# Optimization experiments

Hardware: AMD Instinct MI355X
Metric: run time of the kernel (lower is better)

## Reference

```python
import jax, jax.numpy as jnp
import numpy as np

B, S, NU, ML, H, V = 32, 256, 4, 9, 768, 30522


def setup_inputs() -> dict:
    key = jax.random.key(0)
    ks = jax.random.split(key, 13)
    s = 1.0 / np.sqrt(H)
    return {
        "x": jax.random.randint(ks[0], (B, S), 0, V),
        "decoder_input": jax.random.normal(ks[1], (B, NU, H), jnp.float32) * 0.02,
        "encoder_output": jax.random.normal(ks[2], (B, S, H), jnp.float32) * 0.02,
        "hidden": jax.random.normal(ks[3], (1, B, H), jnp.float32) * 0.02,
        "max_len": ML,
        "teacher": jax.random.randint(ks[4], (B, NU, ML), 0, V),
        "embed_w": jax.random.normal(ks[5], (V, H), jnp.float32) * 0.02,
        "gru_w_ih": jax.random.uniform(ks[6], (3 * H, H), jnp.float32, -s, s),
        "gru_w_hh": jax.random.uniform(ks[7], (3 * H, H), jnp.float32, -s, s),
        "gru_b_ih": jax.random.uniform(ks[8], (3 * H,), jnp.float32, -s, s),
        "gru_b_hh": jax.random.uniform(ks[9], (3 * H,), jnp.float32, -s, s),
        "w_gen_w": jax.random.uniform(ks[10], (1, 3 * H), jnp.float32, -s, s),
        "w_gen_b": jax.random.uniform(ks[11], (1,), jnp.float32, -s, s),
    }


def reference(x, decoder_input, encoder_output, hidden, max_len, teacher,
              embed_w, gru_w_ih, gru_w_hh, gru_b_ih, gru_b_hh, w_gen_w, w_gen_b):
    pad_mask = (x == 0)                       # [B, S]
    b, nu, h_dim = decoder_input.shape
    h0 = hidden[0]                            # [B, H]

    # Teacher-forced input sequence for every (update, step): [NU*ML, B, H]
    tf = embed_w[teacher[:, :, :max_len - 1]]           # [B, NU, ML-1, H]
    tf = jnp.moveaxis(tf, 0, 2)                          # [NU, ML-1, B, H]
    first = jnp.swapaxes(decoder_input, 0, 1)[:, None]   # [NU, 1, B, H]
    ws = jnp.concatenate([first, tf], axis=1).reshape(nu * max_len, b, h_dim)

    def gru_cell(w, h):
        gi = w @ gru_w_ih.T + gru_b_ih        # [B, 3H]
        gh = h @ gru_w_hh.T + gru_b_hh
        i_r, i_z, i_n = jnp.split(gi, 3, axis=-1)
        h_r, h_z, h_n = jnp.split(gh, 3, axis=-1)
        r = jax.nn.sigmoid(i_r + h_r)
        z = jax.nn.sigmoid(i_z + h_z)
        n = jnp.tanh(i_n + r * h_n)
        return (1.0 - z) * n + z * h

    batch_idx = jnp.arange(b)[:, None]

    def step(h, w):
        h = gru_cell(w, h)                                    # [B, H]
        attn_e = jnp.einsum('bsh,bh->bs', encoder_output, h)  # [B, S]
        attn_e = jnp.where(pad_mask, -1e9, attn_e)
        attn_history = jax.nn.softmax(attn_e, axis=-1)        # [B, S]
        attn_vocab = jax.nn.softmax(h @ embed_w.T, axis=-1)   # [B, V]
        context = jnp.einsum('bs,bsh->bh', attn_history, encoder_output)
        gate_in = jnp.concatenate([w, h, context], axis=-1)   # [B, 3H]
        p_gen = jax.nn.sigmoid(gate_in @ w_gen_w.T + w_gen_b) # [B, 1]
        p_ctx = jnp.zeros_like(attn_vocab).at[batch_idx, x].add(attn_history)
        p_final = p_gen * attn_vocab + (1.0 - p_gen) * p_ctx  # [B, V]
        return h, p_final

    _, outs = jax.lax.scan(step, h0, ws)          # [NU*ML, B, V]
    outs = outs.reshape(nu, max_len, b, -1)       # [NU, ML, B, V]
    return jnp.transpose(outs, (2, 0, 1, 3))      # [B, NU, ML, V]
```

## Files before the change

kernel.cpp:

```cpp
#include <hip/hip_runtime.h>
#include <math.h>

#define BB_ 32
#define SS_ 256
#define HH_ 768
#define VV_ 30522
#define TT_ 36
#define MM_ 1152
#define NBLK_GRU 48

typedef __bf16 bf16x8 __attribute__((ext_vector_type(8)));
typedef __bf16 bf16x4 __attribute__((ext_vector_type(4)));
typedef float f32x4 __attribute__((ext_vector_type(4)));

__device__ __forceinline__ float sigmoidf_(float x) { return 1.f / (1.f + expf(-x)); }

__device__ __forceinline__ void async_load16(const void* g, void* l) {
  __builtin_amdgcn_global_load_lds(
      (const __attribute__((address_space(1))) void*)g,
      (__attribute__((address_space(3))) void*)l, 16, 0, 0);
}

__global__ __launch_bounds__(256) void cvt_bf16(const float* __restrict__ s,
                                                __bf16* __restrict__ d, int n4) {
  int i = blockIdx.x * 256 + threadIdx.x;
  if (i < n4) {
    float4 v = reinterpret_cast<const float4*>(s)[i];
    bf16x4 o;
    o[0] = (__bf16)v.x; o[1] = (__bf16)v.y; o[2] = (__bf16)v.z; o[3] = (__bf16)v.w;
    reinterpret_cast<bf16x4*>(d)[i] = o;
  }
}

__global__ __launch_bounds__(256) void build_ws(const float* __restrict__ dec,
                                                const int* __restrict__ teacher,
                                                const float* __restrict__ embed,
                                                __bf16* __restrict__ wsbf) {
  int idx = blockIdx.x * 256 + threadIdx.x;
  if (idx >= MM_ * HH_) return;
  int m = idx / HH_, k = idx - m * HH_;
  int tau = m >> 5, b = m & 31;
  int u = tau / 9, tt = tau - u * 9;
  float v;
  if (tt == 0) v = dec[((size_t)b * 4 + u) * HH_ + k];
  else v = embed[(size_t)teacher[(b * 4 + u) * 9 + tt - 1] * HH_ + k];
  wsbf[idx] = (__bf16)v;
}

__global__ __launch_bounds__(256) void enc_gate(const float* __restrict__ enc,
                                                const float* __restrict__ wgen,
                                                float* __restrict__ encg) {
  int row = blockIdx.x * 4 + (threadIdx.x >> 6);
  int lane = threadIdx.x & 63;
  const float* er = enc + (size_t)row * HH_;
  float ssum = 0.f;
#pragma unroll
  for (int i = 0; i < 12; ++i) ssum += er[i * 64 + lane] * wgen[1536 + i * 64 + lane];
  for (int off = 32; off; off >>= 1) ssum += __shfl_down(ssum, off);
  if (lane == 0) encg[row] = ssum;
}

template <int MODE>
__global__ __launch_bounds__(256) void gemm_bt2(const __bf16* __restrict__ A,
                                                const __bf16* __restrict__ Bm,
                                                float* __restrict__ C,
                                                float* __restrict__ rowsum,
                                                int Nreal, int ldC) {
  __shared__ __bf16 As[128 * 32];
  __shared__ __bf16 Bs[128 * 32];
  const int tid = threadIdx.x;
  const int lane = tid & 63, wave = tid >> 6;
  const int wm = wave >> 1, wn = wave & 1;
  const int q = lane >> 4, ln = lane & 15;
  const int m0 = blockIdx.y * 128, n0 = blockIdx.x * 128;
  const int srow = (wave << 5) + (lane >> 2);
  const int kc = lane & 3;
  const size_t aoff = (size_t)(m0 + srow) * HH_ + kc * 8;
  const size_t aoff2 = aoff + 16 * HH_;
  int br1 = n0 + srow;      if (br1 >= Nreal) br1 = Nreal - 1;
  int br2 = n0 + srow + 16; if (br2 >= Nreal) br2 = Nreal - 1;
  __bf16* lA1 = &As[srow * 32 + kc * 8];
  __bf16* lA2 = &As[(srow + 16) * 32 + kc * 8];
  __bf16* lB1 = &Bs[srow * 32 + kc * 8];
  __bf16* lB2 = &Bs[(srow + 16) * 32 + kc * 8];
  f32x4 acc[4][4] = {};
  for (int kb = 0; kb < 24; ++kb) {
    const int k0 = kb << 5;
    async_load16(A + aoff + k0, lA1);
    async_load16(A + aoff2 + k0, lA2);
    async_load16(Bm + (size_t)br1 * HH_ + kc * 8 + k0, lB1);
    async_load16(Bm + (size_t)br2 * HH_ + kc * 8 + k0, lB2);
    __syncthreads();
    bf16x8 af[4], bfr[4];
#pragma unroll
    for (int mi = 0; mi < 4; ++mi)
      af[mi] = *reinterpret_cast<const bf16x8*>(&As[(wm * 64 + mi * 16 + ln) * 32 + q * 8]);
#pragma unroll
    for (int ni = 0; ni < 4; ++ni)
      bfr[ni] = *reinterpret_cast<const bf16x8*>(&Bs[(wn * 64 + ni * 16 + ln) * 32 + q * 8]);
#pragma unroll
    for (int mi = 0; mi < 4; ++mi)
#pragma unroll
      for (int ni = 0; ni < 4; ++ni)
        acc[mi][ni] = __builtin_amdgcn_mfma_f32_16x16x32_bf16(af[mi], bfr[ni], acc[mi][ni], 0, 0, 0);
    __syncthreads();
  }
#pragma unroll
  for (int mi = 0; mi < 4; ++mi)
#pragma unroll
    for (int r2 = 0; r2 < 4; ++r2) {
      const int m = m0 + wm * 64 + mi * 16 + q * 4 + r2;
      if (MODE == 0) {
#pragma unroll
        for (int ni = 0; ni < 4; ++ni) {
          int n = n0 + wn * 64 + ni * 16 + ln;
          if (n < Nreal) C[(size_t)m * ldC + n] = acc[mi][ni][r2];
        }
      } else {
        float part = 0.f;
#pragma unroll
        for (int ni = 0; ni < 4; ++ni) {
          int n = n0 + wn * 64 + ni * 16 + ln;
          float e = expf(fminf(acc[mi][ni][r2], 60.f));
          if (n < Nreal) { C[(size_t)m * ldC + n] = e; part += e; }
        }
#pragma unroll
        for (int o = 1; o < 16; o <<= 1) part += __shfl_xor(part, o);
        if (ln == 0) atomicAdd(rowsum + m, part);
      }
    }
}

__global__ __launch_bounds__(128) void gru_scan(const __bf16* __restrict__ hid_bf,
                                                const float* __restrict__ H0,
                                                const __bf16* __restrict__ Whh,
                                                const float* __restrict__ GI,
                                                const float* __restrict__ bih,
                                                const float* __restrict__ bhh,
                                                __bf16* __restrict__ Ah,
                                                unsigned* __restrict__ flags) {
  __shared__ __bf16 WhhS[48 * HH_];
  const int tid = threadIdx.x, lane = tid & 63;
  const int mi = tid >> 6;
  const int q = lane >> 4, ln = lane & 15;
  const int jH = blockIdx.x * 16 + ln;
  for (int i = tid; i < 48 * 96; i += 128) {
    int row = i / 96, cs = i - row * 96;
    int g = row >> 4, jl = row & 15;
    bf16x8 v = *reinterpret_cast<const bf16x8*>(
        &Whh[((size_t)(g * 768 + blockIdx.x * 16 + jl)) * HH_ + cs * 8]);
    *reinterpret_cast<bf16x8*>(&WhhS[row * HH_ + ((cs ^ (row & 7)) * 8)]) = v;
  }
  const float bir = bih[jH], biz = bih[jH + 768], bin_ = bih[jH + 1536];
  const float bhr = bhh[jH], bhz = bhh[jH + 768], bhn = bhh[jH + 1536];
  float hc[4];
#pragma unroll
  for (int r2 = 0; r2 < 4; ++r2)
    hc[r2] = H0[(size_t)(mi * 16 + q * 4 + r2) * HH_ + jH];
  const __bf16* w0 = &WhhS[(0 + ln) * HH_];
  const __bf16* w1 = &WhhS[(16 + ln) * HH_];
  const __bf16* w2 = &WhhS[(32 + ln) * HH_];
  const int swz = (ln & 7) * 8;
  __syncthreads();
  for (int tau = 0; tau < TT_; ++tau) {
    const __bf16* arow = tau ? (Ah + ((size_t)(mi * 16 + ln) * TT_ + (tau - 1)) * HH_)
                             : (hid_bf + (size_t)(mi * 16 + ln) * HH_);
    const float* GIt = GI + (size_t)tau * BB_ * 2304;
    float gir[4], giz[4], gin[4];
#pragma unroll
    for (int r2 = 0; r2 < 4; ++r2) {
      const float* gi = GIt + (size_t)(mi * 16 + q * 4 + r2) * 2304;
      gir[r2] = gi[jH]; giz[r2] = gi[jH + 768]; gin[r2] = gi[jH + 1536];
    }
    f32x4 a0 = {}, a1 = {}, a2 = {};
#pragma unroll 4
    for (int kb = 0; kb < 24; ++kb) {
      int k0 = kb * 32 + q * 8;
      int kl = (k0 ^ swz);
      bf16x8 a = *reinterpret_cast<const bf16x8*>(arow + k0);
      bf16x8 b0 = *reinterpret_cast<const bf16x8*>(w0 + kl);
      bf16x8 b1 = *reinterpret_cast<const bf16x8*>(w1 + kl);
      bf16x8 b2 = *reinterpret_cast<const bf16x8*>(w2 + kl);
      a0 = __builtin_amdgcn_mfma_f32_16x16x32_bf16(a, b0, a0, 0, 0, 0);
      a1 = __builtin_amdgcn_mfma_f32_16x16x32_bf16(a, b1, a1, 0, 0, 0);
      a2 = __builtin_amdgcn_mfma_f32_16x16x32_bf16(a, b2, a2, 0, 0, 0);
    }
#pragma unroll
    for (int r2 = 0; r2 < 4; ++r2) {
      int b = mi * 16 + q * 4 + r2;
      float r = sigmoidf_(gir[r2] + bir + a0[r2] + bhr);
      float z = sigmoidf_(giz[r2] + biz + a1[r2] + bhz);
      float n = tanhf(gin[r2] + bin_ + r * (a2[r2] + bhn));
      float h = (1.f - z) * n + z * hc[r2];
      hc[r2] = h;
      Ah[((size_t)b * TT_ + tau) * HH_ + jH] = (__bf16)h;
    }
    if (tau < TT_ - 1) {
      __syncthreads();
      if (tid == 0)
        __hip_atomic_store(&flags[(size_t)blockIdx.x * 16], (unsigned)(tau + 1),
                           __ATOMIC_RELEASE, __HIP_MEMORY_SCOPE_AGENT);
      const unsigned tgt = (unsigned)(tau + 1);
      int ok = 0, spin = 0;
      while (!ok) {
        unsigned v = (lane < NBLK_GRU)
            ? __hip_atomic_load(&flags[(size_t)lane * 16], __ATOMIC_ACQUIRE,
                                __HIP_MEMORY_SCOPE_AGENT)
            : tgt;
        ok = __all((int)(v >= tgt));
        if (!ok) {
          __builtin_amdgcn_s_sleep(1);
          if (++spin > (1 << 20)) break;
        }
      }
    }
  }
}

__global__ __launch_bounds__(256) void attn_gemm(const __bf16* __restrict__ Ah,
                                                 const __bf16* __restrict__ encb,
                                                 float* __restrict__ E) {
  int b = blockIdx.x >> 2, stile = blockIdx.x & 3;
  int wave = threadIdx.x >> 6, lane = threadIdx.x & 63;
  int q = lane >> 4, ln = lane & 15;
  int s = stile * 64 + wave * 16 + ln;
  const __bf16* brow = encb + ((size_t)b * SS_ + s) * HH_;
  const __bf16* arow[3];
#pragma unroll
  for (int mt = 0; mt < 3; ++mt) {
    int tau = mt * 16 + ln; if (tau > 35) tau = 35;
    arow[mt] = Ah + ((size_t)b * TT_ + tau) * HH_;
  }
  f32x4 acc[3] = {};
#pragma unroll 4
  for (int kb = 0; kb < 24; ++kb) {
    int k0 = kb * 32 + q * 8;
    bf16x8 bb = *reinterpret_cast<const bf16x8*>(brow + k0);
#pragma unroll
    for (int mt = 0; mt < 3; ++mt) {
      bf16x8 aa = *reinterpret_cast<const bf16x8*>(arow[mt] + k0);
      acc[mt] = __builtin_amdgcn_mfma_f32_16x16x32_bf16(aa, bb, acc[mt], 0, 0, 0);
    }
  }
#pragma unroll
  for (int mt = 0; mt < 3; ++mt)
#pragma unroll
    for (int r2 = 0; r2 < 4; ++r2) {
      int tau = mt * 16 + q * 4 + r2;
      if (tau < 36) E[((size_t)b * TT_ + tau) * SS_ + s] = acc[mt][r2];
    }
}

__global__ __launch_bounds__(256) void softmax_pg(const float* __restrict__ E,
                                                  const int* __restrict__ x,
                                                  const float* __restrict__ encg,
                                                  const __bf16* __restrict__ wsbf,
                                                  const __bf16* __restrict__ Ah,
                                                  const float* __restrict__ wgen,
                                                  const float* __restrict__ wgenb,
                                                  float* __restrict__ attn,
                                                  float* __restrict__ pg) {
  int m = blockIdx.x;
  int b = m / TT_, tau = m - b * TT_;
  int m_in = tau * 32 + b;
  int t = threadIdx.x;
  __shared__ float red[256];
  __shared__ float r1[256], r2[256], r3[256];
  float e = E[(size_t)m * SS_ + t];
  if (x[b * SS_ + t] == 0) e = -1000000000.0f;
  red[t] = e; __syncthreads();
  for (int off = 128; off; off >>= 1) {
    if (t < off) red[t] = fmaxf(red[t], red[t + off]);
    __syncthreads();
  }
  float mx = red[0];
  float p = expf(e - mx);
  float dsum = 0.f;
#pragma unroll
  for (int i = 0; i < 3; ++i) {
    int k = t + i * 256;
    dsum += (float)wsbf[(size_t)m_in * HH_ + k] * wgen[k];
    dsum += (float)Ah[(size_t)m * HH_ + k] * wgen[768 + k];
  }
  float pe = p * encg[b * SS_ + t];
  r1[t] = p; r2[t] = pe; r3[t] = dsum; __syncthreads();
  for (int off = 128; off; off >>= 1) {
    if (t < off) { r1[t] += r1[t + off]; r2[t] += r2[t + off]; r3[t] += r3[t + off]; }
    __syncthreads();
  }
  float Z = r1[0];
  attn[(size_t)m * SS_ + t] = p / Z;
  if (t == 0) pg[m] = sigmoidf_(r3[0] + r2[0] / Z + wgenb[0]);
}

__global__ __launch_bounds__(256) void finalize(float* __restrict__ C,
                                                const float* __restrict__ rowsum,
                                                const float* __restrict__ pg) {
  int m = blockIdx.y;
  float scale = pg[m] / rowsum[m];
  int base_i = blockIdx.x * 2048;
  size_t rowb = (size_t)m * VV_;
#pragma unroll
  for (int j = 0; j < 8; ++j) {
    int i = base_i + j * 256 + threadIdx.x;
    if (i < VV_) C[rowb + i] *= scale;
  }
}

__global__ __launch_bounds__(256) void scatter_ctx(float* __restrict__ C,
                                                   const float* __restrict__ attn,
                                                   const float* __restrict__ pg,
                                                   const int* __restrict__ x) {
  int m = blockIdx.x, s = threadIdx.x;
  int b = m / TT_;
  float v = (1.f - pg[m]) * attn[(size_t)m * SS_ + s];
  int col = x[b * SS_ + s];
  atomicAdd(C + (size_t)m * VV_ + col, v);
}

extern "C" void kernel_launch(void* const* d_in, const int* in_sizes, int n_in,
                              void* d_out, int out_size, void* d_ws, size_t ws_size,
                              hipStream_t stream) {
  const int*   x       = (const int*)d_in[0];
  const float* dec     = (const float*)d_in[1];
  const float* enc     = (const float*)d_in[2];
  const float* hidden  = (const float*)d_in[3];
  const int*   teacher = (const int*)d_in[5];
  const float* embed   = (const float*)d_in[6];
  const float* wih     = (const float*)d_in[7];
  const float* whh     = (const float*)d_in[8];
  const float* bih     = (const float*)d_in[9];
  const float* bhh     = (const float*)d_in[10];
  const float* wgen    = (const float*)d_in[11];
  const float* wgenb   = (const float*)d_in[12];
  float* out = (float*)d_out;

  char* w = (char*)d_ws;
  __bf16* embed_bf = (__bf16*)w;  w += (size_t)VV_ * HH_ * 2;
  __bf16* enc_bf   = (__bf16*)w;  w += (size_t)BB_ * SS_ * HH_ * 2;
  __bf16* wih_bf   = (__bf16*)w;  w += (size_t)2304 * HH_ * 2;
  __bf16* whh_bf   = (__bf16*)w;  w += (size_t)2304 * HH_ * 2;
  __bf16* ws_bf    = (__bf16*)w;  w += (size_t)MM_ * HH_ * 2;
  __bf16* hid_bf   = (__bf16*)w;  w += (size_t)BB_ * HH_ * 2;
  __bf16* A_h      = (__bf16*)w;  w += (size_t)MM_ * HH_ * 2;
  float*  GI       = (float*)w;   w += (size_t)MM_ * 2304 * 4;
  float*  E        = (float*)w;   w += (size_t)MM_ * SS_ * 4;
  float*  attn     = (float*)w;   w += (size_t)MM_ * SS_ * 4;
  float*  encg     = (float*)w;   w += (size_t)BB_ * SS_ * 4;
  float*  pg       = (float*)w;   w += 8192;
  char*   ctl      = w;           w += 8192;
  float*    rowsum = (float*)ctl;
  unsigned* flags  = (unsigned*)(ctl + 4864);

  hipMemsetAsync(ctl, 0, 8192, stream);

  cvt_bf16<<<(VV_ * HH_ / 4 + 255) / 256, 256, 0, stream>>>(embed, embed_bf, VV_ * HH_ / 4);
  cvt_bf16<<<(BB_ * SS_ * HH_ / 4 + 255) / 256, 256, 0, stream>>>(enc, enc_bf, BB_ * SS_ * HH_ / 4);
  cvt_bf16<<<(2304 * HH_ / 4 + 255) / 256, 256, 0, stream>>>(wih, wih_bf, 2304 * HH_ / 4);
  cvt_bf16<<<(2304 * HH_ / 4 + 255) / 256, 256, 0, stream>>>(whh, whh_bf, 2304 * HH_ / 4);
  cvt_bf16<<<(BB_ * HH_ / 4 + 255) / 256, 256, 0, stream>>>(hidden, hid_bf, BB_ * HH_ / 4);

  build_ws<<<(MM_ * HH_ + 255) / 256, 256, 0, stream>>>(dec, teacher, embed, ws_bf);

  gemm_bt2<0><<<dim3(2304 / 128, MM_ / 128), 256, 0, stream>>>(ws_bf, wih_bf, GI, nullptr, 2304, 2304);

  enc_gate<<<BB_ * SS_ / 4, 256, 0, stream>>>(enc, wgen, encg);

  gru_scan<<<NBLK_GRU, 128, 0, stream>>>(hid_bf, hidden, whh_bf, GI, bih, bhh, A_h, flags);

  attn_gemm<<<BB_ * 4, 256, 0, stream>>>(A_h, enc_bf, E);
  softmax_pg<<<MM_, 256, 0, stream>>>(E, x, encg, ws_bf, A_h, wgen, wgenb, attn, pg);

  gemm_bt2<1><<<dim3((VV_ + 127) / 128, MM_ / 128), 256, 0, stream>>>(A_h, embed_bf, out, rowsum, VV_, VV_);

  finalize<<<dim3((VV_ + 2047) / 2048, MM_), 256, 0, stream>>>(out, rowsum, pg);
  scatter_ctx<<<MM_, 256, 0, stream>>>(out, attn, pg, x);
}
```

Measured before the change: 786.2 us.

## Cut GRU scan step latency with compact exchange buffer and prefetch

The recurrent GRU scan now exchanges the hidden state between blocks through a small double-buffered Hx array, written as packed 32-bit atomic stores, instead of reading back from the strided Ah output. The next step's input-gate values are prefetched before the inter-block spin-wait, the whole A row is loaded into registers before the MFMA loop, and the flag store and load become relaxed with a single acquire fence after the wait. The aim is to shorten the serial per-step critical path of the 36-step scan. Dropping release semantics on the flag store without an explicit release fence could let the Hx stores become visible after the flag, and the larger register footprint adds register pressure.

```diff
diff --git a/kernel.cpp b/kernel.cpp
--- a/kernel.cpp
+++ b/kernel.cpp
@@ -131,14 +131,15 @@
     }
 }
 
-__global__ __launch_bounds__(128) void gru_scan(const __bf16* __restrict__ hid_bf,
-                                                const float* __restrict__ H0,
-                                                const __bf16* __restrict__ Whh,
-                                                const float* __restrict__ GI,
-                                                const float* __restrict__ bih,
-                                                const float* __restrict__ bhh,
-                                                __bf16* __restrict__ Ah,
-                                                unsigned* __restrict__ flags) {
+__global__ __launch_bounds__(128, 1) void gru_scan(const __bf16* __restrict__ hid_bf,
+                                                   const float* __restrict__ H0,
+                                                   const __bf16* __restrict__ Whh,
+                                                   const float* __restrict__ GI,
+                                                   const float* __restrict__ bih,
+                                                   const float* __restrict__ bhh,
+                                                   __bf16* __restrict__ Ah,
+                                                   __bf16* __restrict__ Hx,
+                                                   unsigned* __restrict__ flags) {
   __shared__ __bf16 WhhS[48 * HH_];
   const int tid = threadIdx.x, lane = tid & 63;
   const int mi = tid >> 6;
@@ -161,30 +162,32 @@
   const __bf16* w1 = &WhhS[(16 + ln) * HH_];
   const __bf16* w2 = &WhhS[(32 + ln) * HH_];
   const int swz = (ln & 7) * 8;
+  float gir[4], giz[4], gin[4];
+#pragma unroll
+  for (int r2 = 0; r2 < 4; ++r2) {
+    const float* gi = GI + (size_t)(mi * 16 + q * 4 + r2) * 2304;
+    gir[r2] = gi[jH]; giz[r2] = gi[jH + 768]; gin[r2] = gi[jH + 1536];
+  }
   __syncthreads();
   for (int tau = 0; tau < TT_; ++tau) {
-    const __bf16* arow = tau ? (Ah + ((size_t)(mi * 16 + ln) * TT_ + (tau - 1)) * HH_)
+    const __bf16* arow = tau ? (Hx + (size_t)(((tau - 1) & 1) * 32 + mi * 16 + ln) * HH_)
                              : (hid_bf + (size_t)(mi * 16 + ln) * HH_);
-    const float* GIt = GI + (size_t)tau * BB_ * 2304;
-    float gir[4], giz[4], gin[4];
-#pragma unroll
-    for (int r2 = 0; r2 < 4; ++r2) {
-      const float* gi = GIt + (size_t)(mi * 16 + q * 4 + r2) * 2304;
-      gir[r2] = gi[jH]; giz[r2] = gi[jH + 768]; gin[r2] = gi[jH + 1536];
-    }
+    bf16x8 areg[24];
+#pragma unroll
+    for (int kb = 0; kb < 24; ++kb)
+      areg[kb] = *reinterpret_cast<const bf16x8*>(arow + kb * 32 + q * 8);
     f32x4 a0 = {}, a1 = {}, a2 = {};
-#pragma unroll 4
+#pragma unroll
     for (int kb = 0; kb < 24; ++kb) {
-      int k0 = kb * 32 + q * 8;
-      int kl = (k0 ^ swz);
-      bf16x8 a = *reinterpret_cast<const bf16x8*>(arow + k0);
+      int kl = (kb * 32 + q * 8) ^ swz;
       bf16x8 b0 = *reinterpret_cast<const bf16x8*>(w0 + kl);
       bf16x8 b1 = *reinterpret_cast<const bf16x8*>(w1 + kl);
       bf16x8 b2 = *reinterpret_cast<const bf16x8*>(w2 + kl);
-      a0 = __builtin_amdgcn_mfma_f32_16x16x32_bf16(a, b0, a0, 0, 0, 0);
-      a1 = __builtin_amdgcn_mfma_f32_16x16x32_bf16(a, b1, a1, 0, 0, 0);
-      a2 = __builtin_amdgcn_mfma_f32_16x16x32_bf16(a, b2, a2, 0, 0, 0);
-    }
+      a0 = __builtin_amdgcn_mfma_f32_16x16x32_bf16(areg[kb], b0, a0, 0, 0, 0);
+      a1 = __builtin_amdgcn_mfma_f32_16x16x32_bf16(areg[kb], b1, a1, 0, 0, 0);
+      a2 = __builtin_amdgcn_mfma_f32_16x16x32_bf16(areg[kb], b2, a2, 0, 0, 0);
+    }
+    __bf16* hxc = Hx + (size_t)((tau & 1) * 32) * HH_;
 #pragma unroll
     for (int r2 = 0; r2 < 4; ++r2) {
       int b = mi * 16 + q * 4 + r2;
@@ -193,18 +196,36 @@
       float n = tanhf(gin[r2] + bin_ + r * (a2[r2] + bhn));
       float h = (1.f - z) * n + z * hc[r2];
       hc[r2] = h;
-      Ah[((size_t)b * TT_ + tau) * HH_ + jH] = (__bf16)h;
+      float hp = __shfl_xor(h, 1);
+      __bf16 hb = (__bf16)h, hpb = (__bf16)hp;
+      unsigned lo = (unsigned)__builtin_bit_cast(unsigned short, hb);
+      unsigned hi = (unsigned)__builtin_bit_cast(unsigned short, hpb);
+      if (!(ln & 1)) {
+        unsigned u = lo | (hi << 16);
+        *reinterpret_cast<unsigned*>(&Ah[((size_t)b * TT_ + tau) * HH_ + jH]) = u;
+        if (tau < TT_ - 1)
+          __hip_atomic_store(reinterpret_cast<unsigned*>(&hxc[(size_t)b * HH_ + jH]), u,
+                             __ATOMIC_RELAXED, __HIP_MEMORY_SCOPE_AGENT);
+      }
     }
     if (tau < TT_ - 1) {
       __syncthreads();
       if (tid == 0)
         __hip_atomic_store(&flags[(size_t)blockIdx.x * 16], (unsigned)(tau + 1),
-                           __ATOMIC_RELEASE, __HIP_MEMORY_SCOPE_AGENT);
+                           __ATOMIC_RELAXED, __HIP_MEMORY_SCOPE_AGENT);
+      {
+        const float* GIt = GI + (size_t)(tau + 1) * BB_ * 2304;
+#pragma unroll
+        for (int r2 = 0; r2 < 4; ++r2) {
+          const float* gi = GIt + (size_t)(mi * 16 + q * 4 + r2) * 2304;
+          gir[r2] = gi[jH]; giz[r2] = gi[jH + 768]; gin[r2] = gi[jH + 1536];
+        }
+      }
       const unsigned tgt = (unsigned)(tau + 1);
       int ok = 0, spin = 0;
       while (!ok) {
         unsigned v = (lane < NBLK_GRU)
-            ? __hip_atomic_load(&flags[(size_t)lane * 16], __ATOMIC_ACQUIRE,
+            ? __hip_atomic_load(&flags[(size_t)lane * 16], __ATOMIC_RELAXED,
                                 __HIP_MEMORY_SCOPE_AGENT)
             : tgt;
         ok = __all((int)(v >= tgt));
@@ -213,6 +234,7 @@
           if (++spin > (1 << 20)) break;
         }
       }
+      __builtin_amdgcn_fence(__ATOMIC_ACQUIRE, "agent");
     }
   }
 }
@@ -349,6 +371,7 @@
   float*  encg     = (float*)w;   w += (size_t)BB_ * SS_ * 4;
   float*  pg       = (float*)w;   w += 8192;
   char*   ctl      = w;           w += 8192;
+  __bf16* Hx       = (__bf16*)w;  w += (size_t)2 * BB_ * HH_ * 2;
   float*    rowsum = (float*)ctl;
   unsigned* flags  = (unsigned*)(ctl + 4864);
 
@@ -366,7 +389,7 @@
 
   enc_gate<<<BB_ * SS_ / 4, 256, 0, stream>>>(enc, wgen, encg);
 
-  gru_scan<<<NBLK_GRU, 128, 0, stream>>>(hid_bf, hidden, whh_bf, GI, bih, bhh, A_h, flags);
+  gru_scan<<<NBLK_GRU, 128, 0, stream>>>(hid_bf, hidden, whh_bf, GI, bih, bhh, A_h, Hx, flags);
 
   attn_gemm<<<BB_ * 4, 256, 0, stream>>>(A_h, enc_bf, E);
   softmax_pg<<<MM_, 256, 0, stream>>>(E, x, encg, ws_bf, A_h, wgen, wgenb, attn, pg);
```

After: 769.7 us. 1.02x faster.
